# Optimization experiments

Measured on AMD Instinct MI355X. Metric: run time of the kernel, lower is better.

Reference implementation:

```python
import jax, jax.numpy as jnp
import numpy as np


def setup_inputs() -> dict:
    key = jax.random.key(0)
    k1, k2, k3, k4, k5 = jax.random.split(key, 5)
    B, D, U = 16384, 512, 512
    scale = 1.0 / np.sqrt(D + U)
    return {
        "inputs": jax.random.normal(k1, (B, D), dtype=jnp.float32),
        "h_prev": jax.random.normal(k2, (B, U), dtype=jnp.float32),
        "Wz": jax.random.normal(k3, (D + U, U), dtype=jnp.float32) * scale,
        "Wr": jax.random.normal(k4, (D + U, U), dtype=jnp.float32) * scale,
        "Wh": jax.random.normal(k5, (D + U, U), dtype=jnp.float32) * scale,
    }


def reference(inputs, h_prev, Wz, Wr, Wh):
    # x_h: [B, D+U]
    x_h = jnp.concatenate([inputs, h_prev], axis=-1)
    z = jax.nn.sigmoid(x_h @ Wz)                     # update gate [B, U]
    r = jax.nn.sigmoid(x_h @ Wr)                     # reset gate  [B, U]
    h_hat = jnp.tanh(jnp.concatenate([inputs, r * h_prev], axis=-1) @ Wh)
    new_h = z * h_prev + (1.0 - z) * h_hat
    return new_h
```

## Files before the change

### kernel.cpp

```cpp
#include <hip/hip_runtime.h>
#include <hip/hip_bf16.h>
#include <stdint.h>

typedef __attribute__((ext_vector_type(8))) short short8;
typedef __attribute__((ext_vector_type(4))) float f32x4;
typedef unsigned short u16;

#define AS1 __attribute__((address_space(1)))
#define AS3 __attribute__((address_space(3)))

__device__ __forceinline__ u16 f2b(float f) {
  union { float f; uint32_t u; } c; c.f = f;
  uint32_t u = c.u;
  return (u16)((u + 0x7fffu + ((u >> 16) & 1u)) >> 16);
}
__device__ __forceinline__ float b2f(u16 b) {
  union { uint32_t u; float f; } c; c.u = ((uint32_t)b) << 16;
  return c.f;
}

__global__ void cvt_bf16_kernel(const float* __restrict__ src,
                                u16* __restrict__ dst, int n4) {
  int i = blockIdx.x * blockDim.x + threadIdx.x;
  if (i >= n4) return;
  const float4 v = reinterpret_cast<const float4*>(src)[i];
  ushort4 o;
  o.x = f2b(v.x); o.y = f2b(v.y); o.z = f2b(v.z); o.w = f2b(v.w);
  reinterpret_cast<ushort4*>(dst)[i] = o;
}

__global__ void cvt_transpose_kernel(const float* __restrict__ w0,
                                     const float* __restrict__ w1,
                                     const float* __restrict__ w2,
                                     u16* __restrict__ d0,
                                     u16* __restrict__ d1,
                                     u16* __restrict__ d2,
                                     int K, int N) {
  const float* src = (blockIdx.y == 0) ? w0 : (blockIdx.y == 1 ? w1 : w2);
  u16* dst = (blockIdx.y == 0) ? d0 : (blockIdx.y == 1 ? d1 : d2);
  int idx = blockIdx.x * blockDim.x + threadIdx.x;
  if (idx >= K * N) return;
  int k = idx / N, n = idx - k * N;
  dst[(size_t)n * K + k] = f2b(src[idx]);
}


#define BARO() do { __builtin_amdgcn_s_barrier(); __builtin_amdgcn_sched_barrier(0); } while (0)
#define LGKM0() do { asm volatile("s_waitcnt lgkmcnt(0)" ::: "memory"); __builtin_amdgcn_sched_barrier(0); } while (0)
#define VMW(n) do { asm volatile("s_waitcnt vmcnt(" #n ")" ::: "memory"); __builtin_amdgcn_sched_barrier(0); } while (0)
#define PRIO_MM(MB, NB) do { __builtin_amdgcn_s_setprio(1); mm(MB, NB); __builtin_amdgcn_s_setprio(0); } while (0)

template <int GATES>
__global__ __launch_bounds__(512, 1) void gemm8_kernel(
    const u16* __restrict__ a1,
    const u16* __restrict__ a2,
    const u16* __restrict__ wt,
    const float* __restrict__ hprev,
    const u16* __restrict__ zb_in,
    u16* __restrict__ o_z,
    u16* __restrict__ o_rh,
    float* __restrict__ o_f) {
  constexpr int NT = 16;
  constexpr int NITER = 8;
  constexpr int BN = GATES ? 256 : 128;
  constexpr int MQ = GATES ? 4 : 2;
  constexpr int AHALF = GATES ? 16384 : 8192;
  constexpr int DBUF_E = GATES ? 32768 : 24576;
  constexpr int DB1 = DBUF_E * 2;

  __shared__ u16 lds[2 * DBUF_E];
  const char* ldsb = (const char*)lds;

  const int tid = threadIdx.x;
  const int lane = tid & 63;
  const int wid = tid >> 6;
  const int wm = GATES ? (wid >> 2) : (wid >> 1);
  const int wn = GATES ? (wid & 3) : (wid & 1);

  const int wg = ((int)blockIdx.x & 7) * 32 + ((int)blockIdx.x >> 3);
  const int bn = wg & 3;
  const int bm = wg >> 2;

  const int srow8 = tid >> 3;
  const int swzb = ((tid & 7) ^ (srow8 & 7)) << 4;
  auto STAGE = [&](int t, int kind) {
    if (t >= NT) return;
    u16* dst = lds + (t & 1) * DBUF_E + kind * 8192 + wid * 512;
    if (kind < 2) {
      const char* src = ((t < 8) ? ((const char*)a1 + (size_t)t * 128)
                                 : ((const char*)a2 + (size_t)(t - 8) * 128)) +
                        (size_t)(bm * 256 + kind * 128 + srow8) * 1024 + swzb;
      __builtin_amdgcn_global_load_lds((const AS1 void*)src, (AS3 void*)dst, 16, 0, 0);
      __builtin_amdgcn_global_load_lds((const AS1 void*)(src + 65536), (AS3 void*)(dst + 4096), 16, 0, 0);
    } else {
      const char* src = (const char*)wt +
                        (size_t)(bn * BN + (kind - 2) * 128 + srow8) * 2048 +
                        (size_t)t * 128 + swzb;
      __builtin_amdgcn_global_load_lds((const AS1 void*)src, (AS3 void*)dst, 16, 0, 0);
      __builtin_amdgcn_global_load_lds((const AS1 void*)(src + 131072), (AS3 void*)(dst + 4096), 16, 0, 0);
    }
  };

  const int rsel = lane & 15;
  const int kg = lane >> 4;
  const int sl0 = (kg ^ (rsel & 7)) << 4;
  const int sl1 = ((4 + kg) ^ (rsel & 7)) << 4;
  const int aoff0 = wm * AHALF + rsel * 128;
  const int boff0 = 32768 + wn * 8192 + rsel * 128;

  f32x4 acc[2 * MQ][4] = {};
  short8 a[MQ][2], b[4][2];

  auto ldA = [&](int DB, int mfb) {
#pragma unroll
    for (int mi = 0; mi < MQ; ++mi) {
      a[mi][0] = *(const short8*)(ldsb + DB + aoff0 + (mfb + mi) * 2048 + sl0);
      a[mi][1] = *(const short8*)(ldsb + DB + aoff0 + (mfb + mi) * 2048 + sl1);
    }
  };
  auto ldB = [&](int DB, int nfb) {
#pragma unroll
    for (int ni = 0; ni < 2; ++ni) {
      b[nfb + ni][0] = *(const short8*)(ldsb + DB + boff0 + (nfb + ni) * 2048 + sl0);
      b[nfb + ni][1] = *(const short8*)(ldsb + DB + boff0 + (nfb + ni) * 2048 + sl1);
    }
  };
  auto mm = [&](int mb, int nb) {
#pragma unroll
    for (int mi = 0; mi < MQ; ++mi)
#pragma unroll
      for (int ni = 0; ni < 2; ++ni) {
        acc[mb + mi][nb + ni] = __builtin_amdgcn_mfma_f32_16x16x32_bf16(a[mi][0], b[nb + ni][0], acc[mb + mi][nb + ni], 0, 0, 0);
        acc[mb + mi][nb + ni] = __builtin_amdgcn_mfma_f32_16x16x32_bf16(a[mi][1], b[nb + ni][1], acc[mb + mi][nb + ni], 0, 0, 0);
      }
  };

  if constexpr (GATES) {
    STAGE(0, 2); STAGE(0, 3); STAGE(0, 0); STAGE(0, 1); STAGE(1, 2); STAGE(1, 3);
    VMW(4);
  } else {
    STAGE(0, 2); STAGE(0, 0); STAGE(0, 1); STAGE(1, 2);
    VMW(2);
  }
  BARO();

  for (int j = 0; j < NITER; ++j) {
    const int t1 = 2 * j + 1, t2 = 2 * j + 2, t3 = 2 * j + 3;
    ldA(0, 0); ldB(0, 0); STAGE(t1, 0);
    BARO(); LGKM0(); PRIO_MM(0, 0); BARO();
    ldB(0, 2); STAGE(t1, 1);
    BARO(); LGKM0(); PRIO_MM(0, 2); BARO();
    ldA(0, MQ); STAGE(t2, 2);
    BARO(); LGKM0(); PRIO_MM(MQ, 2); BARO();
    if constexpr (GATES) STAGE(t2, 3); else STAGE(t2, 0);
    BARO(); PRIO_MM(MQ, 0);
    if (j == NITER - 1) { VMW(0); } else { VMW(4); }
    BARO();
    ldA(DB1, 0); ldB(DB1, 0);
    if constexpr (GATES) STAGE(t2, 0); else STAGE(t2, 1);
    BARO(); LGKM0(); PRIO_MM(0, 0); BARO();
    ldB(DB1, 2);
    if constexpr (GATES) STAGE(t2, 1);
    BARO(); LGKM0(); PRIO_MM(0, 2); BARO();
    ldA(DB1, MQ); STAGE(t3, 2);
    BARO(); LGKM0(); PRIO_MM(MQ, 2); BARO();
    if constexpr (GATES) STAGE(t3, 3);
    BARO(); PRIO_MM(MQ, 0);
    if (j == NITER - 1) { VMW(0); }
    else { if constexpr (GATES) VMW(4); else VMW(2); }
    BARO();
  }

  const int row0 = bm * 256 + wm * (GATES ? 128 : 64) + kg * 4;
  const int col0 = bn * BN + wn * 64 + rsel;
  if constexpr (GATES) {
    if (bn < 2) {
#pragma unroll
      for (int mf = 0; mf < 8; ++mf)
#pragma unroll
        for (int nf = 0; nf < 4; ++nf)
#pragma unroll
          for (int q = 0; q < 4; ++q) {
            const int row = row0 + mf * 16 + q;
            const int col = col0 + nf * 16;
            const float zf = 1.f / (1.f + __expf(-acc[mf][nf][q]));
            o_z[(size_t)row * 512 + col] = f2b(zf);
          }
    } else {
#pragma unroll
      for (int mf = 0; mf < 8; ++mf)
#pragma unroll
        for (int nf = 0; nf < 4; ++nf)
#pragma unroll
          for (int q = 0; q < 4; ++q) {
            const int row = row0 + mf * 16 + q;
            const int col = col0 + nf * 16 - 512;
            const size_t idx = (size_t)row * 512 + col;
            const float rf = 1.f / (1.f + __expf(-acc[mf][nf][q]));
            o_rh[idx] = f2b(rf * hprev[idx]);
          }
    }
  } else {
#pragma unroll
    for (int mf = 0; mf < 4; ++mf)
#pragma unroll
      for (int nf = 0; nf < 4; ++nf)
#pragma unroll
        for (int q = 0; q < 4; ++q) {
          const int row = row0 + mf * 16 + q;
          const int col = col0 + nf * 16;
          const size_t idx = (size_t)row * 512 + col;
          const float s = acc[mf][nf][q];
          const float hh = 2.f / (1.f + __expf(-2.f * s)) - 1.f;
          const float z = b2f(zb_in[idx]);
          o_f[idx] = z * hprev[idx] + (1.f - z) * hh;
        }
  }
}

extern "C" void kernel_launch(void* const* d_in, const int* in_sizes, int n_in,
                              void* d_out, int out_size, void* d_ws, size_t ws_size,
                              hipStream_t stream) {
  const float* inputs = (const float*)d_in[0];
  const float* h_prev = (const float*)d_in[1];
  const float* Wz = (const float*)d_in[2];
  const float* Wr = (const float*)d_in[3];
  const float* Wh = (const float*)d_in[4];
  float* out = (float*)d_out;

  const int B = 16384, D = 512, U = 512, K = 1024;

  u16* xb = (u16*)d_ws;
  u16* hb = xb + (size_t)B * D;
  u16* wzt = hb + (size_t)B * U;
  u16* wrt = wzt + (size_t)K * U;
  u16* wht = wrt + (size_t)K * U;
  u16* zb = wht + (size_t)K * U;
  u16* rhb = zb + (size_t)B * U;

  const int n4 = (B * D) / 4;
  cvt_bf16_kernel<<<(n4 + 255) / 256, 256, 0, stream>>>(inputs, xb, n4);
  cvt_bf16_kernel<<<(n4 + 255) / 256, 256, 0, stream>>>(h_prev, hb, n4);
  dim3 tg((K * U + 255) / 256, 3);
  cvt_transpose_kernel<<<tg, 256, 0, stream>>>(Wz, Wr, Wh, wzt, wrt, wht, K, U);

  gemm8_kernel<1><<<dim3(256), 512, 0, stream>>>(xb, hb, wzt, h_prev, nullptr, zb, rhb, nullptr);
  gemm8_kernel<0><<<dim3(256), 512, 0, stream>>>(xb, rhb, wht, h_prev, zb, nullptr, nullptr, out);
}
```

Before: 99.49 us.

## Double-buffer LDS fragment registers and read bf16 h_prev in epilogues

Restructures the GEMM main loop so LDS fragment reads for the next MFMA block go into alternate register sets (aA/aB, bA/bB/bC) and are issued before the current block's MFMAs. This lets LDS reads overlap compute, and the global-to-LDS staging is reordered around the barriers, including a deeper prologue that stages two k-tiles. The epilogues now read h_prev from the bf16 copy instead of fp32, which halves those reads but adds bf16 rounding error to the z*h_prev term of the final output. Register pressure rises because of the extra fragment buffers.

```diff
diff --git a/kernel.cpp b/kernel.cpp
--- a/kernel.cpp
+++ b/kernel.cpp
@@ -45,17 +45,17 @@
 }
 
 
-#define BARO() do { __builtin_amdgcn_s_barrier(); __builtin_amdgcn_sched_barrier(0); } while (0)
+#define BAR() do { __builtin_amdgcn_s_barrier(); __builtin_amdgcn_sched_barrier(0); } while (0)
+#define SB() __builtin_amdgcn_sched_barrier(0)
 #define LGKM0() do { asm volatile("s_waitcnt lgkmcnt(0)" ::: "memory"); __builtin_amdgcn_sched_barrier(0); } while (0)
 #define VMW(n) do { asm volatile("s_waitcnt vmcnt(" #n ")" ::: "memory"); __builtin_amdgcn_sched_barrier(0); } while (0)
-#define PRIO_MM(MB, NB) do { __builtin_amdgcn_s_setprio(1); mm(MB, NB); __builtin_amdgcn_s_setprio(0); } while (0)
 
 template <int GATES>
 __global__ __launch_bounds__(512, 1) void gemm8_kernel(
     const u16* __restrict__ a1,
     const u16* __restrict__ a2,
     const u16* __restrict__ wt,
-    const float* __restrict__ hprev,
+    const u16* __restrict__ hb,
     const u16* __restrict__ zb_in,
     u16* __restrict__ o_z,
     u16* __restrict__ o_rh,
@@ -66,7 +66,7 @@
   constexpr int MQ = GATES ? 4 : 2;
   constexpr int AHALF = GATES ? 16384 : 8192;
   constexpr int DBUF_E = GATES ? 32768 : 24576;
-  constexpr int DB1 = DBUF_E * 2;
+  constexpr int DB1B = DBUF_E * 2;
 
   __shared__ u16 lds[2 * DBUF_E];
   const char* ldsb = (const char*)lds;
@@ -109,66 +109,78 @@
   const int boff0 = 32768 + wn * 8192 + rsel * 128;
 
   f32x4 acc[2 * MQ][4] = {};
-  short8 a[MQ][2], b[4][2];
-
-  auto ldA = [&](int DB, int mfb) {
+  short8 aA[MQ][2], aB[MQ][2];
+  short8 bA[2][2], bB[2][2], bC[2][2];
+
+  auto RD_A = [&](auto& dst, int DB, int mfb) {
 #pragma unroll
     for (int mi = 0; mi < MQ; ++mi) {
-      a[mi][0] = *(const short8*)(ldsb + DB + aoff0 + (mfb + mi) * 2048 + sl0);
-      a[mi][1] = *(const short8*)(ldsb + DB + aoff0 + (mfb + mi) * 2048 + sl1);
-    }
-  };
-  auto ldB = [&](int DB, int nfb) {
+      dst[mi][0] = *(const short8*)(ldsb + DB + aoff0 + (mfb + mi) * 2048 + sl0);
+      dst[mi][1] = *(const short8*)(ldsb + DB + aoff0 + (mfb + mi) * 2048 + sl1);
+    }
+  };
+  auto RD_B = [&](auto& dst, int DB, int nfb) {
 #pragma unroll
     for (int ni = 0; ni < 2; ++ni) {
-      b[nfb + ni][0] = *(const short8*)(ldsb + DB + boff0 + (nfb + ni) * 2048 + sl0);
-      b[nfb + ni][1] = *(const short8*)(ldsb + DB + boff0 + (nfb + ni) * 2048 + sl1);
-    }
-  };
-  auto mm = [&](int mb, int nb) {
+      dst[ni][0] = *(const short8*)(ldsb + DB + boff0 + (nfb + ni) * 2048 + sl0);
+      dst[ni][1] = *(const short8*)(ldsb + DB + boff0 + (nfb + ni) * 2048 + sl1);
+    }
+  };
+  auto MM = [&](auto& A, auto& Bv, int mb, int nb) {
+    __builtin_amdgcn_s_setprio(1);
 #pragma unroll
     for (int mi = 0; mi < MQ; ++mi)
 #pragma unroll
       for (int ni = 0; ni < 2; ++ni) {
-        acc[mb + mi][nb + ni] = __builtin_amdgcn_mfma_f32_16x16x32_bf16(a[mi][0], b[nb + ni][0], acc[mb + mi][nb + ni], 0, 0, 0);
-        acc[mb + mi][nb + ni] = __builtin_amdgcn_mfma_f32_16x16x32_bf16(a[mi][1], b[nb + ni][1], acc[mb + mi][nb + ni], 0, 0, 0);
+        acc[mb + mi][nb + ni] = __builtin_amdgcn_mfma_f32_16x16x32_bf16(A[mi][0], Bv[ni][0], acc[mb + mi][nb + ni], 0, 0, 0);
+        acc[mb + mi][nb + ni] = __builtin_amdgcn_mfma_f32_16x16x32_bf16(A[mi][1], Bv[ni][1], acc[mb + mi][nb + ni], 0, 0, 0);
       }
-  };
-
-  if constexpr (GATES) {
-    STAGE(0, 2); STAGE(0, 3); STAGE(0, 0); STAGE(0, 1); STAGE(1, 2); STAGE(1, 3);
-    VMW(4);
-  } else {
-    STAGE(0, 2); STAGE(0, 0); STAGE(0, 1); STAGE(1, 2);
-    VMW(2);
-  }
-  BARO();
-
+    __builtin_amdgcn_s_setprio(0);
+  };
+
+  STAGE(0, 2); if constexpr (GATES) STAGE(0, 3);
+  STAGE(0, 0); STAGE(0, 1);
+  STAGE(1, 2); if constexpr (GATES) STAGE(1, 3);
+  STAGE(1, 0); STAGE(1, 1);
+  if constexpr (GATES) VMW(8); else VMW(6);
+  BAR();
+  RD_A(aA, 0, 0); RD_B(bA, 0, 0);
+
+#pragma unroll 1
   for (int j = 0; j < NITER; ++j) {
-    const int t1 = 2 * j + 1, t2 = 2 * j + 2, t3 = 2 * j + 3;
-    ldA(0, 0); ldB(0, 0); STAGE(t1, 0);
-    BARO(); LGKM0(); PRIO_MM(0, 0); BARO();
-    ldB(0, 2); STAGE(t1, 1);
-    BARO(); LGKM0(); PRIO_MM(0, 2); BARO();
-    ldA(0, MQ); STAGE(t2, 2);
-    BARO(); LGKM0(); PRIO_MM(MQ, 2); BARO();
-    if constexpr (GATES) STAGE(t2, 3); else STAGE(t2, 0);
-    BARO(); PRIO_MM(MQ, 0);
-    if (j == NITER - 1) { VMW(0); } else { VMW(4); }
-    BARO();
-    ldA(DB1, 0); ldB(DB1, 0);
-    if constexpr (GATES) STAGE(t2, 0); else STAGE(t2, 1);
-    BARO(); LGKM0(); PRIO_MM(0, 0); BARO();
-    ldB(DB1, 2);
-    if constexpr (GATES) STAGE(t2, 1);
-    BARO(); LGKM0(); PRIO_MM(0, 2); BARO();
-    ldA(DB1, MQ); STAGE(t3, 2);
-    BARO(); LGKM0(); PRIO_MM(MQ, 2); BARO();
-    if constexpr (GATES) STAGE(t3, 3);
-    BARO(); PRIO_MM(MQ, 0);
-    if (j == NITER - 1) { VMW(0); }
-    else { if constexpr (GATES) VMW(4); else VMW(2); }
-    BARO();
+    const int e2 = 2 * j + 2, o2 = 2 * j + 3;
+    const bool stg = e2 < NT;
+    LGKM0(); RD_B(bC, 0, 2); SB();
+    MM(aA, bA, 0, 0); BAR();
+    LGKM0(); RD_A(aB, 0, MQ); SB();
+    MM(aA, bC, 0, 2); BAR();
+    LGKM0();
+    if (stg) { STAGE(e2, 2); if constexpr (GATES) STAGE(e2, 3); }
+    SB();
+    MM(aB, bC, MQ, 2);
+    if (stg) { if constexpr (GATES) VMW(4); else VMW(2); } else VMW(0);
+    BAR();
+    LGKM0(); RD_A(aA, DB1B, 0); RD_B(bB, DB1B, 0);
+    if (stg) STAGE(e2, 0);
+    SB();
+    MM(aB, bA, MQ, 0); BAR();
+    LGKM0(); RD_B(bC, DB1B, 2);
+    if (stg) STAGE(e2, 1);
+    SB();
+    MM(aA, bB, 0, 0); BAR();
+    LGKM0(); RD_A(aB, DB1B, MQ); SB();
+    MM(aA, bC, 0, 2); BAR();
+    LGKM0();
+    if (o2 < NT) STAGE(o2, 2);
+    SB();
+    MM(aB, bC, MQ, 2);
+    if (stg) VMW(2); else VMW(0);
+    BAR();
+    LGKM0();
+    if (j < NITER - 1) { RD_A(aA, 0, 0); RD_B(bA, 0, 0); }
+    if (o2 < NT) { if constexpr (GATES) STAGE(o2, 3); STAGE(o2, 0); STAGE(o2, 1); }
+    SB();
+    MM(aB, bB, MQ, 0); BAR();
   }
 
   const int row0 = bm * 256 + wm * (GATES ? 128 : 64) + kg * 4;
@@ -197,7 +209,7 @@
             const int col = col0 + nf * 16 - 512;
             const size_t idx = (size_t)row * 512 + col;
             const float rf = 1.f / (1.f + __expf(-acc[mf][nf][q]));
-            o_rh[idx] = f2b(rf * hprev[idx]);
+            o_rh[idx] = f2b(rf * b2f(hb[idx]));
           }
     }
   } else {
@@ -213,7 +225,7 @@
           const float s = acc[mf][nf][q];
           const float hh = 2.f / (1.f + __expf(-2.f * s)) - 1.f;
           const float z = b2f(zb_in[idx]);
-          o_f[idx] = z * hprev[idx] + (1.f - z) * hh;
+          o_f[idx] = z * b2f(hb[idx]) + (1.f - z) * hh;
         }
   }
 }
@@ -244,6 +256,6 @@
   dim3 tg((K * U + 255) / 256, 3);
   cvt_transpose_kernel<<<tg, 256, 0, stream>>>(Wz, Wr, Wh, wzt, wrt, wht, K, U);
 
-  gemm8_kernel<1><<<dim3(256), 512, 0, stream>>>(xb, hb, wzt, h_prev, nullptr, zb, rhb, nullptr);
-  gemm8_kernel<0><<<dim3(256), 512, 0, stream>>>(xb, rhb, wht, h_prev, zb, nullptr, nullptr, out);
-}
+  gemm8_kernel<1><<<dim3(256), 512, 0, stream>>>(xb, hb, wzt, hb, nullptr, zb, rhb, nullptr);
+  gemm8_kernel<0><<<dim3(256), 512, 0, stream>>>(xb, rhb, wht, hb, zb, nullptr, nullptr, out);
+}
```

After: 119.8 us. +20.5%, slower.

## Split GEMM template into gate and candidate kernels with deeper A-tile buffering

Applied to the files above, without the earlier changes.

The shared template is replaced by two specialised kernels. The candidate kernel gets a new LDS layout: the B tile shares its buffer while the A tiles rotate through three regions, so staging runs further ahead of compute. The epilogues now read the bf16 copy of h_prev instead of the fp32 one, which halves that traffic at a small precision cost. The MFMA issue order is changed to loop over k-slices outermost, and the main loops are marked unroll 1.

```diff
diff --git a/kernel.cpp b/kernel.cpp
--- a/kernel.cpp
+++ b/kernel.cpp
@@ -44,57 +44,39 @@
   dst[(size_t)n * K + k] = f2b(src[idx]);
 }
 
-
-#define BARO() do { __builtin_amdgcn_s_barrier(); __builtin_amdgcn_sched_barrier(0); } while (0)
+#define BAR() do { __builtin_amdgcn_s_barrier(); __builtin_amdgcn_sched_barrier(0); } while (0)
 #define LGKM0() do { asm volatile("s_waitcnt lgkmcnt(0)" ::: "memory"); __builtin_amdgcn_sched_barrier(0); } while (0)
 #define VMW(n) do { asm volatile("s_waitcnt vmcnt(" #n ")" ::: "memory"); __builtin_amdgcn_sched_barrier(0); } while (0)
-#define PRIO_MM(MB, NB) do { __builtin_amdgcn_s_setprio(1); mm(MB, NB); __builtin_amdgcn_s_setprio(0); } while (0)
-
-template <int GATES>
-__global__ __launch_bounds__(512, 1) void gemm8_kernel(
-    const u16* __restrict__ a1,
-    const u16* __restrict__ a2,
+
+__global__ __launch_bounds__(512, 1) void gemm_gates_kernel(
+    const u16* __restrict__ xb, const u16* __restrict__ hb,
     const u16* __restrict__ wt,
-    const float* __restrict__ hprev,
-    const u16* __restrict__ zb_in,
-    u16* __restrict__ o_z,
-    u16* __restrict__ o_rh,
-    float* __restrict__ o_f) {
-  constexpr int NT = 16;
-  constexpr int NITER = 8;
-  constexpr int BN = GATES ? 256 : 128;
-  constexpr int MQ = GATES ? 4 : 2;
-  constexpr int AHALF = GATES ? 16384 : 8192;
-  constexpr int DBUF_E = GATES ? 32768 : 24576;
-  constexpr int DB1 = DBUF_E * 2;
-
-  __shared__ u16 lds[2 * DBUF_E];
+    u16* __restrict__ o_z, u16* __restrict__ o_rh) {
+  constexpr int NT = 16, NITER = 8;
+  __shared__ u16 lds[65536];
   const char* ldsb = (const char*)lds;
 
   const int tid = threadIdx.x;
   const int lane = tid & 63;
   const int wid = tid >> 6;
-  const int wm = GATES ? (wid >> 2) : (wid >> 1);
-  const int wn = GATES ? (wid & 3) : (wid & 1);
-
+  const int wm = wid >> 2, wn = wid & 3;
   const int wg = ((int)blockIdx.x & 7) * 32 + ((int)blockIdx.x >> 3);
-  const int bn = wg & 3;
-  const int bm = wg >> 2;
+  const int bn = wg & 3, bm = wg >> 2;
 
   const int srow8 = tid >> 3;
   const int swzb = ((tid & 7) ^ (srow8 & 7)) << 4;
   auto STAGE = [&](int t, int kind) {
     if (t >= NT) return;
-    u16* dst = lds + (t & 1) * DBUF_E + kind * 8192 + wid * 512;
+    u16* dst = lds + (t & 1) * 32768 + kind * 8192 + wid * 512;
     if (kind < 2) {
-      const char* src = ((t < 8) ? ((const char*)a1 + (size_t)t * 128)
-                                 : ((const char*)a2 + (size_t)(t - 8) * 128)) +
+      const char* src = ((t < 8) ? ((const char*)xb + (size_t)t * 128)
+                                 : ((const char*)hb + (size_t)(t - 8) * 128)) +
                         (size_t)(bm * 256 + kind * 128 + srow8) * 1024 + swzb;
       __builtin_amdgcn_global_load_lds((const AS1 void*)src, (AS3 void*)dst, 16, 0, 0);
       __builtin_amdgcn_global_load_lds((const AS1 void*)(src + 65536), (AS3 void*)(dst + 4096), 16, 0, 0);
     } else {
       const char* src = (const char*)wt +
-                        (size_t)(bn * BN + (kind - 2) * 128 + srow8) * 2048 +
+                        (size_t)(bn * 256 + (kind - 2) * 128 + srow8) * 2048 +
                         (size_t)t * 128 + swzb;
       __builtin_amdgcn_global_load_lds((const AS1 void*)src, (AS3 void*)dst, 16, 0, 0);
       __builtin_amdgcn_global_load_lds((const AS1 void*)(src + 131072), (AS3 void*)(dst + 4096), 16, 0, 0);
@@ -105,15 +87,15 @@
   const int kg = lane >> 4;
   const int sl0 = (kg ^ (rsel & 7)) << 4;
   const int sl1 = ((4 + kg) ^ (rsel & 7)) << 4;
-  const int aoff0 = wm * AHALF + rsel * 128;
+  const int aoff0 = wm * 16384 + rsel * 128;
   const int boff0 = 32768 + wn * 8192 + rsel * 128;
 
-  f32x4 acc[2 * MQ][4] = {};
-  short8 a[MQ][2], b[4][2];
+  f32x4 acc[8][4] = {};
+  short8 a[4][2], b[4][2];
 
   auto ldA = [&](int DB, int mfb) {
 #pragma unroll
-    for (int mi = 0; mi < MQ; ++mi) {
+    for (int mi = 0; mi < 4; ++mi) {
       a[mi][0] = *(const short8*)(ldsb + DB + aoff0 + (mfb + mi) * 2048 + sl0);
       a[mi][1] = *(const short8*)(ldsb + DB + aoff0 + (mfb + mi) * 2048 + sl1);
     }
@@ -125,97 +107,193 @@
       b[nfb + ni][1] = *(const short8*)(ldsb + DB + boff0 + (nfb + ni) * 2048 + sl1);
     }
   };
-  auto mm = [&](int mb, int nb) {
-#pragma unroll
-    for (int mi = 0; mi < MQ; ++mi)
-#pragma unroll
-      for (int ni = 0; ni < 2; ++ni) {
-        acc[mb + mi][nb + ni] = __builtin_amdgcn_mfma_f32_16x16x32_bf16(a[mi][0], b[nb + ni][0], acc[mb + mi][nb + ni], 0, 0, 0);
-        acc[mb + mi][nb + ni] = __builtin_amdgcn_mfma_f32_16x16x32_bf16(a[mi][1], b[nb + ni][1], acc[mb + mi][nb + ni], 0, 0, 0);
-      }
-  };
-
-  if constexpr (GATES) {
-    STAGE(0, 2); STAGE(0, 3); STAGE(0, 0); STAGE(0, 1); STAGE(1, 2); STAGE(1, 3);
-    VMW(4);
-  } else {
-    STAGE(0, 2); STAGE(0, 0); STAGE(0, 1); STAGE(1, 2);
-    VMW(2);
-  }
-  BARO();
-
+  auto MM = [&](int mb, int nb) {
+    __builtin_amdgcn_s_setprio(1);
+#pragma unroll
+    for (int ks = 0; ks < 2; ++ks)
+#pragma unroll
+      for (int mi = 0; mi < 4; ++mi)
+#pragma unroll
+        for (int ni = 0; ni < 2; ++ni)
+          acc[mb + mi][nb + ni] = __builtin_amdgcn_mfma_f32_16x16x32_bf16(
+              a[mi][ks], b[nb + ni][ks], acc[mb + mi][nb + ni], 0, 0, 0);
+    __builtin_amdgcn_s_setprio(0);
+  };
+
+  STAGE(0, 2); STAGE(0, 3); STAGE(0, 0); STAGE(0, 1); STAGE(1, 2); STAGE(1, 3);
+  VMW(4); BAR();
+
+#pragma unroll 1
   for (int j = 0; j < NITER; ++j) {
     const int t1 = 2 * j + 1, t2 = 2 * j + 2, t3 = 2 * j + 3;
     ldA(0, 0); ldB(0, 0); STAGE(t1, 0);
-    BARO(); LGKM0(); PRIO_MM(0, 0); BARO();
+    BAR(); LGKM0(); MM(0, 0); BAR();
     ldB(0, 2); STAGE(t1, 1);
-    BARO(); LGKM0(); PRIO_MM(0, 2); BARO();
-    ldA(0, MQ); STAGE(t2, 2);
-    BARO(); LGKM0(); PRIO_MM(MQ, 2); BARO();
-    if constexpr (GATES) STAGE(t2, 3); else STAGE(t2, 0);
-    BARO(); PRIO_MM(MQ, 0);
+    BAR(); LGKM0(); MM(0, 2); BAR();
+    ldA(0, 4); STAGE(t2, 2);
+    BAR(); LGKM0(); MM(4, 2); BAR();
+    STAGE(t2, 3);
+    BAR(); MM(4, 0);
     if (j == NITER - 1) { VMW(0); } else { VMW(4); }
-    BARO();
-    ldA(DB1, 0); ldB(DB1, 0);
-    if constexpr (GATES) STAGE(t2, 0); else STAGE(t2, 1);
-    BARO(); LGKM0(); PRIO_MM(0, 0); BARO();
-    ldB(DB1, 2);
-    if constexpr (GATES) STAGE(t2, 1);
-    BARO(); LGKM0(); PRIO_MM(0, 2); BARO();
-    ldA(DB1, MQ); STAGE(t3, 2);
-    BARO(); LGKM0(); PRIO_MM(MQ, 2); BARO();
-    if constexpr (GATES) STAGE(t3, 3);
-    BARO(); PRIO_MM(MQ, 0);
-    if (j == NITER - 1) { VMW(0); }
-    else { if constexpr (GATES) VMW(4); else VMW(2); }
-    BARO();
+    BAR();
+    ldA(65536, 0); ldB(65536, 0); STAGE(t2, 0);
+    BAR(); LGKM0(); MM(0, 0); BAR();
+    ldB(65536, 2); STAGE(t2, 1);
+    BAR(); LGKM0(); MM(0, 2); BAR();
+    ldA(65536, 4); STAGE(t3, 2);
+    BAR(); LGKM0(); MM(4, 2); BAR();
+    STAGE(t3, 3);
+    BAR(); MM(4, 0);
+    if (j == NITER - 1) { VMW(0); } else { VMW(4); }
+    BAR();
   }
 
-  const int row0 = bm * 256 + wm * (GATES ? 128 : 64) + kg * 4;
-  const int col0 = bn * BN + wn * 64 + rsel;
-  if constexpr (GATES) {
-    if (bn < 2) {
-#pragma unroll
-      for (int mf = 0; mf < 8; ++mf)
-#pragma unroll
-        for (int nf = 0; nf < 4; ++nf)
-#pragma unroll
-          for (int q = 0; q < 4; ++q) {
-            const int row = row0 + mf * 16 + q;
-            const int col = col0 + nf * 16;
-            const float zf = 1.f / (1.f + __expf(-acc[mf][nf][q]));
-            o_z[(size_t)row * 512 + col] = f2b(zf);
-          }
-    } else {
-#pragma unroll
-      for (int mf = 0; mf < 8; ++mf)
-#pragma unroll
-        for (int nf = 0; nf < 4; ++nf)
-#pragma unroll
-          for (int q = 0; q < 4; ++q) {
-            const int row = row0 + mf * 16 + q;
-            const int col = col0 + nf * 16 - 512;
-            const size_t idx = (size_t)row * 512 + col;
-            const float rf = 1.f / (1.f + __expf(-acc[mf][nf][q]));
-            o_rh[idx] = f2b(rf * hprev[idx]);
-          }
-    }
-  } else {
-#pragma unroll
-    for (int mf = 0; mf < 4; ++mf)
+  const int row0 = bm * 256 + wm * 128 + kg * 4;
+  const int col0 = bn * 256 + wn * 64 + rsel;
+  if (bn < 2) {
+#pragma unroll
+    for (int mf = 0; mf < 8; ++mf)
 #pragma unroll
       for (int nf = 0; nf < 4; ++nf)
 #pragma unroll
         for (int q = 0; q < 4; ++q) {
           const int row = row0 + mf * 16 + q;
           const int col = col0 + nf * 16;
+          const float zf = 1.f / (1.f + __expf(-acc[mf][nf][q]));
+          o_z[(size_t)row * 512 + col] = f2b(zf);
+        }
+  } else {
+#pragma unroll
+    for (int mf = 0; mf < 8; ++mf)
+#pragma unroll
+      for (int nf = 0; nf < 4; ++nf)
+#pragma unroll
+        for (int q = 0; q < 4; ++q) {
+          const int row = row0 + mf * 16 + q;
+          const int col = col0 + nf * 16 - 512;
           const size_t idx = (size_t)row * 512 + col;
-          const float s = acc[mf][nf][q];
-          const float hh = 2.f / (1.f + __expf(-2.f * s)) - 1.f;
-          const float z = b2f(zb_in[idx]);
-          o_f[idx] = z * hprev[idx] + (1.f - z) * hh;
+          const float rf = 1.f / (1.f + __expf(-acc[mf][nf][q]));
+          o_rh[idx] = f2b(rf * b2f(hb[idx]));
         }
   }
+}
+
+__global__ __launch_bounds__(512, 1) void gemm_cand_kernel(
+    const u16* __restrict__ xb, const u16* __restrict__ rhb,
+    const u16* __restrict__ wt, const u16* __restrict__ hb,
+    const u16* __restrict__ zb_in, float* __restrict__ o_f) {
+  constexpr int NT = 16;
+  __shared__ u16 lds[73728];
+  const char* ldsb = (const char*)lds;
+
+  const int tid = threadIdx.x;
+  const int lane = tid & 63;
+  const int wid = tid >> 6;
+  const int wm = wid >> 2, wn = wid & 3;
+  const int wg = ((int)blockIdx.x & 7) * 32 + ((int)blockIdx.x >> 3);
+  const int bn = wg & 3, bm = wg >> 2;
+
+  const int srow8 = tid >> 3;
+  const int swzb = ((tid & 7) ^ (srow8 & 7)) << 4;
+  auto STG_A = [&](int t, int half, int regionByte) {
+    if (t >= NT) return;
+    u16* dst = lds + regionByte / 2 + half * 8192 + wid * 512;
+    const char* src = ((t < 8) ? ((const char*)xb + (size_t)t * 128)
+                               : ((const char*)rhb + (size_t)(t - 8) * 128)) +
+                      (size_t)(bm * 256 + half * 128 + srow8) * 1024 + swzb;
+    __builtin_amdgcn_global_load_lds((const AS1 void*)src, (AS3 void*)dst, 16, 0, 0);
+    __builtin_amdgcn_global_load_lds((const AS1 void*)(src + 65536), (AS3 void*)(dst + 4096), 16, 0, 0);
+  };
+  auto STG_B = [&](int t, int regionByte) {
+    if (t >= NT) return;
+    u16* dst = lds + regionByte / 2 + wid * 512;
+    const char* src = (const char*)wt + (size_t)(bn * 128 + srow8) * 2048 +
+                      (size_t)t * 128 + swzb;
+    __builtin_amdgcn_global_load_lds((const AS1 void*)src, (AS3 void*)dst, 16, 0, 0);
+    __builtin_amdgcn_global_load_lds((const AS1 void*)(src + 131072), (AS3 void*)(dst + 4096), 16, 0, 0);
+  };
+
+  const int rsel = lane & 15;
+  const int kg = lane >> 4;
+  const int sl0 = (kg ^ (rsel & 7)) << 4;
+  const int sl1 = ((4 + kg) ^ (rsel & 7)) << 4;
+  const int aoff0 = wm * 16384 + rsel * 128;
+  const int boff0 = wn * 4096 + rsel * 128;
+
+  f32x4 acc[8][2] = {};
+  short8 a[4][2], b[2][2];
+
+  auto RD_A = [&](int regionByte, int mfb) {
+#pragma unroll
+    for (int mi = 0; mi < 4; ++mi) {
+      a[mi][0] = *(const short8*)(ldsb + regionByte + aoff0 + (mfb + mi) * 2048 + sl0);
+      a[mi][1] = *(const short8*)(ldsb + regionByte + aoff0 + (mfb + mi) * 2048 + sl1);
+    }
+  };
+  auto RD_B = [&](int regionByte) {
+#pragma unroll
+    for (int ni = 0; ni < 2; ++ni) {
+      b[ni][0] = *(const short8*)(ldsb + regionByte + boff0 + ni * 2048 + sl0);
+      b[ni][1] = *(const short8*)(ldsb + regionByte + boff0 + ni * 2048 + sl1);
+    }
+  };
+  auto MM = [&](int mb) {
+    __builtin_amdgcn_s_setprio(1);
+#pragma unroll
+    for (int ks = 0; ks < 2; ++ks)
+#pragma unroll
+      for (int mi = 0; mi < 4; ++mi)
+#pragma unroll
+        for (int ni = 0; ni < 2; ++ni)
+          acc[mb + mi][ni] = __builtin_amdgcn_mfma_f32_16x16x32_bf16(
+              a[mi][ks], b[ni][ks], acc[mb + mi][ni], 0, 0, 0);
+    __builtin_amdgcn_s_setprio(0);
+  };
+
+  STG_B(0, 32768); STG_A(0, 0, 0); STG_A(0, 1, 0);
+  STG_A(1, 0, 49152); STG_A(1, 1, 49152); STG_B(1, 114688);
+  VMW(6); BAR();
+
+  auto ITER = [&](int j, int pr, bool last) {
+    const int e2 = 2 * j + 2, o2 = 2 * j + 3;
+    const int OA = 49152 + pr * 32768, OAs = 49152 + (1 - pr) * 32768;
+    const int OB = 114688 + pr * 16384, OBs = 114688 + (1 - pr) * 16384;
+    RD_A(0, 0); RD_B(32768); STG_A(o2, 0, OAs);
+    BAR(); LGKM0(); MM(0); BAR();
+    RD_A(0, 4); STG_A(o2, 1, OAs); STG_B(e2, 32768);
+    BAR(); LGKM0(); MM(4);
+    if (last) { VMW(0); } else { VMW(6); }
+    BAR();
+    RD_A(OA, 0); RD_B(OB); STG_A(e2, 0, 0); STG_A(e2, 1, 0); STG_B(o2, OBs);
+    BAR(); LGKM0(); MM(0); BAR();
+    RD_A(OA, 4);
+    BAR(); LGKM0(); MM(4);
+    if (last) { VMW(0); } else { VMW(2); }
+    BAR();
+  };
+
+#pragma unroll 1
+  for (int jj = 0; jj < 4; ++jj) {
+    ITER(2 * jj, 0, false);
+    ITER(2 * jj + 1, 1, jj == 3);
+  }
+
+  const int row0 = bm * 256 + wm * 128 + kg * 4;
+  const int col0 = bn * 128 + wn * 32 + rsel;
+#pragma unroll
+  for (int mf = 0; mf < 8; ++mf)
+#pragma unroll
+    for (int nf = 0; nf < 2; ++nf)
+#pragma unroll
+      for (int q = 0; q < 4; ++q) {
+        const int row = row0 + mf * 16 + q;
+        const int col = col0 + nf * 16;
+        const size_t idx = (size_t)row * 512 + col;
+        const float s = acc[mf][nf][q];
+        const float hh = 2.f / (1.f + __expf(-2.f * s)) - 1.f;
+        const float z = b2f(zb_in[idx]);
+        o_f[idx] = z * b2f(hb[idx]) + (1.f - z) * hh;
+      }
 }
 
 extern "C" void kernel_launch(void* const* d_in, const int* in_sizes, int n_in,
@@ -244,6 +322,6 @@
   dim3 tg((K * U + 255) / 256, 3);
   cvt_transpose_kernel<<<tg, 256, 0, stream>>>(Wz, Wr, Wh, wzt, wrt, wht, K, U);
 
-  gemm8_kernel<1><<<dim3(256), 512, 0, stream>>>(xb, hb, wzt, h_prev, nullptr, zb, rhb, nullptr);
-  gemm8_kernel<0><<<dim3(256), 512, 0, stream>>>(xb, rhb, wht, h_prev, zb, nullptr, nullptr, out);
-}
+  gemm_gates_kernel<<<dim3(256), 512, 0, stream>>>(xb, hb, wzt, zb, rhb);
+  gemm_cand_kernel<<<dim3(256), 512, 0, stream>>>(xb, rhb, wht, hb, zb, out);
+}
```

Result: slower. 101.9 us (+2.4%).
